# Kernel optimization log

Measured on AMD Instinct MI355X. Metric: run time of the kernel, lower is better.

The kernel has to match this reference:

```python
import jax, jax.numpy as jnp
import numpy as np

N = 8192      # num_nodes (adj.shape[0])
CIN = 32
COUT = 32     # must equal CIN so wd = x @ wp @ x.T is (N, N)
CS = 4        # Chebyshev order, static operator
CD = 4        # Chebyshev order, dynamic operator


def setup_inputs() -> dict:
    key = jax.random.key(0)
    k1, k2, k3, k4, k5 = jax.random.split(key, 5)
    x = jax.random.normal(k1, (N, CIN), jnp.float32)
    # scale ws so its spectral radius is O(1); keeps the Chebyshev recurrence numerically tame
    ws = jax.random.normal(k2, (N, N), jnp.float32) * np.float32(1.0 / np.sqrt(N))
    # small scale on wp so wd = x wp x^T has O(1) entries
    wp = jax.random.normal(k3, (CIN, COUT), jnp.float32) * np.float32(1e-3)
    ts = jax.random.normal(k4, (CS, CIN, COUT), jnp.float32)
    td = jax.random.normal(k5, (CD, CIN, COUT), jnp.float32)
    return {"x": x, "ws": ws, "wp": wp, "ts": ts, "td": td}


def reference(x, ws, wp, ts, td):
    # Static operator: Chebyshev expansion T0 = I, T1 = ws, Tk = 2 ws T_{k-1} - T_{k-2}.
    # Run the recurrence on the propagated features y_k = T_k(ws) @ x  (N, cin)
    # instead of forming the (N, N) polynomial matrices -- same math, far less traffic.
    y0 = x                      # T0 @ x
    y1 = ws @ x                 # T1 @ x
    out = y0 @ ts[0]            # shared k=0 term (added into both branches, as in the source)
    out_s = out + y1 @ ts[1]
    for k in range(2, CS):
        y0, y1 = y1, 2.0 * (ws @ y1) - y0
        out_s = out_s + y1 @ ts[k]
    # Dynamic operator: data-dependent graph wd = x @ wp @ x.T  (N, N)
    wd = (x @ wp) @ x.T
    z0 = x
    z1 = wd @ x
    out_d = out + z1 @ td[1]
    for k in range(2, CD):
        z0, z1 = z1, 2.0 * (wd @ z1) - z0
        out_d = out_d + z1 @ td[k]
    # act_func is None in this configuration
    return out_s + out_d
```

## Files before the change

kernel.cpp:

```cpp
#include <hip/hip_runtime.h>
#include <hip/hip_bf16.h>


typedef __attribute__((ext_vector_type(8))) short short8;
typedef __attribute__((ext_vector_type(4))) float floatx4;

__device__ inline unsigned short f2bf(float f) {
    union { float f; unsigned u; } v; v.f = f;
    unsigned r = v.u + 0x7FFFu + ((v.u >> 16) & 1u);
    return (unsigned short)(r >> 16);
}

__global__ __launch_bounds__(256) void k_prep(const float* __restrict__ x,
                                              const float* __restrict__ wp,
                                              float* __restrict__ xp,
                                              float* __restrict__ Gpart,
                                              unsigned short* __restrict__ Vt) {
    __shared__ float sx[8192];
    __shared__ float swp[1024];
    __shared__ unsigned short st[32][264];
    const int t = threadIdx.x;
    const int n0 = blockIdx.x * 256;
    const floatx4* x4 = (const floatx4*)(x + (size_t)n0 * 32);
    floatx4* sx4 = (floatx4*)sx;
#pragma unroll
    for (int i = 0; i < 8; ++i) sx4[i * 256 + t] = x4[i * 256 + t];
    for (int i = t; i < 1024; i += 256) swp[i] = wp[i];
    __syncthreads();

    float row[32];
#pragma unroll
    for (int a = 0; a < 32; ++a) row[a] = sx[t * 32 + a];

    float* xpr = xp + (size_t)(n0 + t) * 32;
#pragma unroll
    for (int c = 0; c < 32; ++c) {
        float s = 0.f;
#pragma unroll
        for (int a = 0; a < 32; ++a) s += row[a] * swp[a * 32 + c];
        xpr[c] = s;
        st[c][t] = f2bf(row[c]);
    }

    const int a = t >> 3;
    const int b = 4 * (t & 7);
    float g0 = 0.f, g1 = 0.f, g2 = 0.f, g3 = 0.f;
    for (int i = 0; i < 256; ++i) {
        float va = sx[i * 32 + a];
        floatx4 vb = *(floatx4*)&sx[i * 32 + b];
        g0 += va * vb.x; g1 += va * vb.y; g2 += va * vb.z; g3 += va * vb.w;
    }
    floatx4 g = {g0, g1, g2, g3};
    *(floatx4*)&Gpart[(size_t)blockIdx.x * 1024 + (size_t)(a * 32 + b)] = g;

    __syncthreads();
#pragma unroll
    for (int c = 0; c < 32; ++c) Vt[(size_t)c * 8192 + n0 + t] = st[c][t];
}

__global__ void k_coef(const float* __restrict__ Gpart, const float* __restrict__ wp,
                       const float* __restrict__ ts, const float* __restrict__ td,
                       float* __restrict__ Cx, float* __restrict__ Cxp) {
    __shared__ float G[1024], W[1024], H1[1024], H2[1024];
    __shared__ float swp[1024], td1[1024], td2[1024], td3[1024], ts0[1024];
    int t = threadIdx.x;
    int a = t >> 5, b = t & 31;
    float gs = 0.f;
    for (int p = 0; p < 32; ++p) gs += Gpart[p * 1024 + t];
    G[t] = gs; swp[t] = wp[t]; ts0[t] = ts[t];
    td1[t] = td[1024 + t]; td2[t] = td[2048 + t]; td3[t] = td[3072 + t];
    __syncthreads();
    float s = 0.f;
    for (int c = 0; c < 32; ++c) s += G[a * 32 + c] * swp[c * 32 + b];
    W[t] = s; __syncthreads();
    s = 0.f;
    for (int c = 0; c < 32; ++c) s += W[a * 32 + c] * G[c * 32 + b];
    H1[t] = s; __syncthreads();
    s = 0.f;
    for (int c = 0; c < 32; ++c) s += W[a * 32 + c] * H1[c * 32 + b];
    H2[t] = 2.f * s - G[t]; __syncthreads();
    s = 0.f;
    for (int c = 0; c < 32; ++c)
        s += G[a * 32 + c] * td1[c * 32 + b]
           + 2.f * H1[a * 32 + c] * td2[c * 32 + b]
           + (2.f * H2[a * 32 + c] - G[a * 32 + c]) * td3[c * 32 + b];
    Cxp[t] = s;
    Cx[t] = 2.f * ts0[t] - td2[t];
}

template <bool CONV>
__global__ __launch_bounds__(256) void k_gemm(const float* __restrict__ Af,
                                              const unsigned short* __restrict__ Ab,
                                              unsigned short* __restrict__ wsb_out,
                                              const unsigned short* __restrict__ Vt,
                                              float* __restrict__ Ypart) {
    const int t = threadIdx.x;
    const int lane = t & 63;
    const int wv = t >> 6;
    const int l15 = lane & 15;
    const int l4 = lane >> 4;
    const int m0 = blockIdx.x * 64;
    const int k0 = blockIdx.y * 1024;

    floatx4 acc0 = {0.f, 0.f, 0.f, 0.f};
    floatx4 acc1 = {0.f, 0.f, 0.f, 0.f};

    if (CONV) {
        __shared__ float sm[64 * 64];
        for (int kt = 0; kt < 1024; kt += 64) {
            __syncthreads();
#pragma unroll
            for (int i = 0; i < 4; ++i) {
                int r = i * 16 + (t >> 4);
                int j = t & 15;
                int cch = j ^ (r & 15);
                const float* gsrc = Af + (size_t)(m0 + r) * 8192 + (k0 + kt) + cch * 4;
                float* ldst = &sm[(i * 16 + wv * 4) * 64];
                __builtin_amdgcn_global_load_lds(
                    (const __attribute__((address_space(1))) unsigned int*)gsrc,
                    (__attribute__((address_space(3))) unsigned int*)ldst, 16, 0, 0);
            }
            __syncthreads();
#pragma unroll
            for (int kh = 0; kh < 2; ++kh) {
                int rl = wv * 16 + l15;
                int jb = kh * 8 + l4 * 2;
                floatx4 f0 = *(floatx4*)&sm[rl * 64 + ((jb    ) ^ l15) * 4];
                floatx4 f1 = *(floatx4*)&sm[rl * 64 + ((jb + 1) ^ l15) * 4];
                short8 av;
                av[0] = f2bf(f0.x); av[1] = f2bf(f0.y); av[2] = f2bf(f0.z); av[3] = f2bf(f0.w);
                av[4] = f2bf(f1.x); av[5] = f2bf(f1.y); av[6] = f2bf(f1.z); av[7] = f2bf(f1.w);
                int kk = k0 + kt + kh * 32 + l4 * 8;
                *(short8*)(wsb_out + (size_t)(m0 + rl) * 8192 + kk) = av;
                short8 b0 = *(const short8*)(Vt + (size_t)l15 * 8192 + kk);
                short8 b1 = *(const short8*)(Vt + (size_t)(16 + l15) * 8192 + kk);
                acc0 = __builtin_amdgcn_mfma_f32_16x16x32_bf16(av, b0, acc0, 0, 0, 0);
                acc1 = __builtin_amdgcn_mfma_f32_16x16x32_bf16(av, b1, acc1, 0, 0, 0);
            }
        }
    } else {
        __shared__ unsigned short sm16[64 * 64];
        for (int kt = 0; kt < 1024; kt += 64) {
            __syncthreads();
#pragma unroll
            for (int i = 0; i < 2; ++i) {
                int r = i * 32 + (t >> 3);
                int j = t & 7;
                int cch = j ^ (r & 7);
                const unsigned short* gsrc =
                    Ab + (size_t)(m0 + r) * 8192 + (k0 + kt) + cch * 8;
                unsigned short* ldst = &sm16[(i * 32 + wv * 8) * 64];
                __builtin_amdgcn_global_load_lds(
                    (const __attribute__((address_space(1))) unsigned int*)gsrc,
                    (__attribute__((address_space(3))) unsigned int*)ldst, 16, 0, 0);
            }
            __syncthreads();
#pragma unroll
            for (int kh = 0; kh < 2; ++kh) {
                int rl = wv * 16 + l15;
                short8 av = *(short8*)&sm16[rl * 64 + ((kh * 4 + l4) ^ (rl & 7)) * 8];
                int kk = k0 + kt + kh * 32 + l4 * 8;
                short8 b0 = *(const short8*)(Vt + (size_t)l15 * 8192 + kk);
                short8 b1 = *(const short8*)(Vt + (size_t)(16 + l15) * 8192 + kk);
                acc0 = __builtin_amdgcn_mfma_f32_16x16x32_bf16(av, b0, acc0, 0, 0, 0);
                acc1 = __builtin_amdgcn_mfma_f32_16x16x32_bf16(av, b1, acc1, 0, 0, 0);
            }
        }
    }
    float* yp = Ypart + (size_t)blockIdx.y * 262144;
    int row0 = m0 + wv * 16 + l4 * 4;
#pragma unroll
    for (int i = 0; i < 4; ++i) {
        yp[(size_t)(row0 + i) * 32 + l15] = acc0[i];
        yp[(size_t)(row0 + i) * 32 + 16 + l15] = acc1[i];
    }
}

__global__ __launch_bounds__(256) void k_trans(const float* __restrict__ Ypart,
                                               const float* __restrict__ prev,
                                               float alpha, float beta,
                                               float* __restrict__ y,
                                               unsigned short* __restrict__ Vt) {
    __shared__ unsigned short st[32][264];
    const int t = threadIdx.x;
    const int n0 = blockIdx.x * 256;
    const size_t base4 = (size_t)n0 * 8;
    floatx4 r[8];
#pragma unroll
    for (int j = 0; j < 8; ++j) r[j] = {0.f, 0.f, 0.f, 0.f};
    for (int p = 0; p < 8; ++p) {
        const floatx4* P4 = (const floatx4*)(Ypart + (size_t)p * 262144);
#pragma unroll
        for (int j = 0; j < 8; ++j) r[j] += P4[base4 + j * 256 + t];
    }
    const floatx4* prev4 = (const floatx4*)prev;
    floatx4* y4 = (floatx4*)y;
#pragma unroll
    for (int j = 0; j < 8; ++j) {
        floatx4 pv = prev4[base4 + j * 256 + t];
        floatx4 v;
        v.x = alpha * r[j].x + beta * pv.x;
        v.y = alpha * r[j].y + beta * pv.y;
        v.z = alpha * r[j].z + beta * pv.z;
        v.w = alpha * r[j].w + beta * pv.w;
        y4[base4 + j * 256 + t] = v;
        int q = j * 256 + t;
        int lr = q >> 3;
        int c4 = (q & 7) * 4;
        st[c4 + 0][lr] = f2bf(v.x);
        st[c4 + 1][lr] = f2bf(v.y);
        st[c4 + 2][lr] = f2bf(v.z);
        st[c4 + 3][lr] = f2bf(v.w);
    }
    __syncthreads();
#pragma unroll
    for (int c = 0; c < 32; ++c) Vt[(size_t)c * 8192 + n0 + t] = st[c][t];
}

__global__ void k_final(const float* __restrict__ x, const float* __restrict__ xp,
                        const float* __restrict__ y1, const float* __restrict__ y2,
                        const float* __restrict__ y3, const float* __restrict__ Cx,
                        const float* __restrict__ Cxp, const float* __restrict__ ts,
                        float* __restrict__ out) {
    __shared__ float m0[1024], m1[1024], m2[1024], m3[1024], m4[1024];
    int t = threadIdx.x;
    for (int i = t; i < 1024; i += 256) {
        m0[i] = Cx[i]; m1[i] = Cxp[i];
        m2[i] = ts[1024 + i]; m3[i] = ts[2048 + i]; m4[i] = ts[3072 + i];
    }
    __syncthreads();
    int g = blockIdx.x * 256 + t;
    int n = g >> 5, c = g & 31;
    const float* xr  = x  + (size_t)n * 32;
    const float* xpr = xp + (size_t)n * 32;
    const float* y1r = y1 + (size_t)n * 32;
    const float* y2r = y2 + (size_t)n * 32;
    const float* y3r = y3 + (size_t)n * 32;
    float s = 0.f;
#pragma unroll
    for (int a = 0; a < 32; ++a) {
        s += xr[a]  * m0[a * 32 + c]
           + xpr[a] * m1[a * 32 + c]
           + y1r[a] * m2[a * 32 + c]
           + y2r[a] * m3[a * 32 + c]
           + y3r[a] * m4[a * 32 + c];
    }
    out[g] = s;
}

extern "C" void kernel_launch(void* const* d_in, const int* in_sizes, int n_in,
                              void* d_out, int out_size, void* d_ws, size_t ws_size,
                              hipStream_t stream) {
    const float* x  = (const float*)d_in[0];
    const float* ws = (const float*)d_in[1];
    const float* wp = (const float*)d_in[2];
    const float* ts = (const float*)d_in[3];
    const float* td = (const float*)d_in[4];
    float* out = (float*)d_out;

    char* w = (char*)d_ws;
    unsigned short* wsb = (unsigned short*)w;
    float* Ppart = (float*)(w + 134217728);
    float* xp  = Ppart + 2097152;
    float* y1  = xp + 262144;
    float* y2  = y1 + 262144;
    float* y3  = y2 + 262144;
    unsigned short* Vt = (unsigned short*)(y3 + 262144);
    float* Gpart = (float*)(Vt + 262144);
    float* Cx  = Gpart + 32768;
    float* Cxp = Cx + 1024;

    dim3 gg(128, 8);
    k_prep<<<32, 256, 0, stream>>>(x, wp, xp, Gpart, Vt);
    k_coef<<<1, 1024, 0, stream>>>(Gpart, wp, ts, td, Cx, Cxp);
    k_gemm<true><<<gg, 256, 0, stream>>>(ws, nullptr, wsb, Vt, Ppart);
    k_trans<<<32, 256, 0, stream>>>(Ppart, x, 1.0f, 0.0f, y1, Vt);
    k_gemm<false><<<gg, 256, 0, stream>>>(nullptr, wsb, nullptr, Vt, Ppart);
    k_trans<<<32, 256, 0, stream>>>(Ppart, x, 2.0f, -1.0f, y2, Vt);
    k_gemm<false><<<gg, 256, 0, stream>>>(nullptr, wsb, nullptr, Vt, Ppart);
    k_trans<<<32, 256, 0, stream>>>(Ppart, y1, 2.0f, -1.0f, y3, Vt);

    k_final<<<1024, 256, 0, stream>>>(x, xp, y1, y2, y3, Cx, Cxp, ts, out);
}
```

Baseline: 567.3 us.

## Store bf16 ws in MFMA-fragment order and drop LDS staging in GEMMs

The first GEMM now reads fp32 ws rows directly from global memory with no LDS or barriers, converts them to bf16, and writes them out in a per-block, per-wave fragment-ordered layout. The later GEMMs can then load each lane's A fragment as one fully coalesced 16-byte read with no shared memory. The K split is doubled to 16 to raise the number of blocks in flight. In exchange, the reduction kernel reads twice as many partial buffers, and the fp32 row reads in the first GEMM are strided rather than cooperatively staged.

```diff
diff --git a/kernel.cpp b/kernel.cpp
--- a/kernel.cpp
+++ b/kernel.cpp
@@ -4,6 +4,9 @@
 
 typedef __attribute__((ext_vector_type(8))) short short8;
 typedef __attribute__((ext_vector_type(4))) float floatx4;
+
+constexpr int NSPLIT = 16;
+constexpr int KT_PER = 8;
 
 __device__ inline unsigned short f2bf(float f) {
     union { float f; unsigned u; } v; v.f = f;
@@ -88,91 +91,91 @@
     Cx[t] = 2.f * ts0[t] - td2[t];
 }
 
-template <bool CONV>
-__global__ __launch_bounds__(256) void k_gemm(const float* __restrict__ Af,
-                                              const unsigned short* __restrict__ Ab,
-                                              unsigned short* __restrict__ wsb_out,
-                                              const unsigned short* __restrict__ Vt,
-                                              float* __restrict__ Ypart) {
+__global__ __launch_bounds__(256) void k_gemm1(const float* __restrict__ A,
+                                               unsigned short* __restrict__ wsb,
+                                               const unsigned short* __restrict__ Vt,
+                                               float* __restrict__ Ypart) {
     const int t = threadIdx.x;
     const int lane = t & 63;
     const int wv = t >> 6;
     const int l15 = lane & 15;
     const int l4 = lane >> 4;
-    const int m0 = blockIdx.x * 64;
-    const int k0 = blockIdx.y * 1024;
+    const int bx = blockIdx.x, by = blockIdx.y;
+    const int k0 = by * 512;
+    const int row = bx * 64 + wv * 16 + l15;
+
+    const float* arow = A + (size_t)row * 8192 + k0 + l4 * 8;
+    unsigned short* wout =
+        wsb + (((size_t)(bx * NSPLIT + by) * 4096) + (size_t)wv * 64 + lane) * 8;
+    const unsigned short* vb0 = Vt + (size_t)l15 * 8192 + k0 + l4 * 8;
+    const unsigned short* vb1 = vb0 + (size_t)16 * 8192;
 
     floatx4 acc0 = {0.f, 0.f, 0.f, 0.f};
     floatx4 acc1 = {0.f, 0.f, 0.f, 0.f};
 
-    if (CONV) {
-        __shared__ float sm[64 * 64];
-        for (int kt = 0; kt < 1024; kt += 64) {
-            __syncthreads();
-#pragma unroll
-            for (int i = 0; i < 4; ++i) {
-                int r = i * 16 + (t >> 4);
-                int j = t & 15;
-                int cch = j ^ (r & 15);
-                const float* gsrc = Af + (size_t)(m0 + r) * 8192 + (k0 + kt) + cch * 4;
-                float* ldst = &sm[(i * 16 + wv * 4) * 64];
-                __builtin_amdgcn_global_load_lds(
-                    (const __attribute__((address_space(1))) unsigned int*)gsrc,
-                    (__attribute__((address_space(3))) unsigned int*)ldst, 16, 0, 0);
-            }
-            __syncthreads();
-#pragma unroll
-            for (int kh = 0; kh < 2; ++kh) {
-                int rl = wv * 16 + l15;
-                int jb = kh * 8 + l4 * 2;
-                floatx4 f0 = *(floatx4*)&sm[rl * 64 + ((jb    ) ^ l15) * 4];
-                floatx4 f1 = *(floatx4*)&sm[rl * 64 + ((jb + 1) ^ l15) * 4];
-                short8 av;
-                av[0] = f2bf(f0.x); av[1] = f2bf(f0.y); av[2] = f2bf(f0.z); av[3] = f2bf(f0.w);
-                av[4] = f2bf(f1.x); av[5] = f2bf(f1.y); av[6] = f2bf(f1.z); av[7] = f2bf(f1.w);
-                int kk = k0 + kt + kh * 32 + l4 * 8;
-                *(short8*)(wsb_out + (size_t)(m0 + rl) * 8192 + kk) = av;
-                short8 b0 = *(const short8*)(Vt + (size_t)l15 * 8192 + kk);
-                short8 b1 = *(const short8*)(Vt + (size_t)(16 + l15) * 8192 + kk);
-                acc0 = __builtin_amdgcn_mfma_f32_16x16x32_bf16(av, b0, acc0, 0, 0, 0);
-                acc1 = __builtin_amdgcn_mfma_f32_16x16x32_bf16(av, b1, acc1, 0, 0, 0);
-            }
+#pragma unroll
+    for (int kt = 0; kt < KT_PER; ++kt) {
+#pragma unroll
+        for (int i = 0; i < 2; ++i) {
+            const int kk = kt * 64 + i * 32;
+            floatx4 f0 = *(const floatx4*)(arow + kk);
+            floatx4 f1 = *(const floatx4*)(arow + kk + 4);
+            short8 av;
+            av[0] = f2bf(f0.x); av[1] = f2bf(f0.y); av[2] = f2bf(f0.z); av[3] = f2bf(f0.w);
+            av[4] = f2bf(f1.x); av[5] = f2bf(f1.y); av[6] = f2bf(f1.z); av[7] = f2bf(f1.w);
+            *(short8*)(wout + (size_t)(kt * 2 + i) * 2048) = av;
+            short8 b0 = *(const short8*)(vb0 + kk);
+            short8 b1 = *(const short8*)(vb1 + kk);
+            acc0 = __builtin_amdgcn_mfma_f32_16x16x32_bf16(av, b0, acc0, 0, 0, 0);
+            acc1 = __builtin_amdgcn_mfma_f32_16x16x32_bf16(av, b1, acc1, 0, 0, 0);
         }
-    } else {
-        __shared__ unsigned short sm16[64 * 64];
-        for (int kt = 0; kt < 1024; kt += 64) {
-            __syncthreads();
-#pragma unroll
-            for (int i = 0; i < 2; ++i) {
-                int r = i * 32 + (t >> 3);
-                int j = t & 7;
-                int cch = j ^ (r & 7);
-                const unsigned short* gsrc =
-                    Ab + (size_t)(m0 + r) * 8192 + (k0 + kt) + cch * 8;
-                unsigned short* ldst = &sm16[(i * 32 + wv * 8) * 64];
-                __builtin_amdgcn_global_load_lds(
-                    (const __attribute__((address_space(1))) unsigned int*)gsrc,
-                    (__attribute__((address_space(3))) unsigned int*)ldst, 16, 0, 0);
-            }
-            __syncthreads();
-#pragma unroll
-            for (int kh = 0; kh < 2; ++kh) {
-                int rl = wv * 16 + l15;
-                short8 av = *(short8*)&sm16[rl * 64 + ((kh * 4 + l4) ^ (rl & 7)) * 8];
-                int kk = k0 + kt + kh * 32 + l4 * 8;
-                short8 b0 = *(const short8*)(Vt + (size_t)l15 * 8192 + kk);
-                short8 b1 = *(const short8*)(Vt + (size_t)(16 + l15) * 8192 + kk);
-                acc0 = __builtin_amdgcn_mfma_f32_16x16x32_bf16(av, b0, acc0, 0, 0, 0);
-                acc1 = __builtin_amdgcn_mfma_f32_16x16x32_bf16(av, b1, acc1, 0, 0, 0);
-            }
+    }
+    float* yp = Ypart + (size_t)by * 262144;
+    const int row0 = bx * 64 + wv * 16 + l4 * 4;
+#pragma unroll
+    for (int r = 0; r < 4; ++r) {
+        yp[(size_t)(row0 + r) * 32 + l15] = acc0[r];
+        yp[(size_t)(row0 + r) * 32 + 16 + l15] = acc1[r];
+    }
+}
+
+__global__ __launch_bounds__(256) void k_gemm2(const unsigned short* __restrict__ wsb,
+                                               const unsigned short* __restrict__ Vt,
+                                               float* __restrict__ Ypart) {
+    const int t = threadIdx.x;
+    const int lane = t & 63;
+    const int wv = t >> 6;
+    const int l15 = lane & 15;
+    const int l4 = lane >> 4;
+    const int bx = blockIdx.x, by = blockIdx.y;
+    const int k0 = by * 512;
+
+    const short8* win = (const short8*)wsb
+        + ((size_t)(bx * NSPLIT + by) * 4096) + (size_t)wv * 64 + lane;
+    const unsigned short* vb0 = Vt + (size_t)l15 * 8192 + k0 + l4 * 8;
+    const unsigned short* vb1 = vb0 + (size_t)16 * 8192;
+
+    floatx4 acc0 = {0.f, 0.f, 0.f, 0.f};
+    floatx4 acc1 = {0.f, 0.f, 0.f, 0.f};
+
+#pragma unroll
+    for (int kt = 0; kt < KT_PER; ++kt) {
+#pragma unroll
+        for (int i = 0; i < 2; ++i) {
+            const int kk = kt * 64 + i * 32;
+            short8 av = win[(size_t)(kt * 2 + i) * 256];
+            short8 b0 = *(const short8*)(vb0 + kk);
+            short8 b1 = *(const short8*)(vb1 + kk);
+            acc0 = __builtin_amdgcn_mfma_f32_16x16x32_bf16(av, b0, acc0, 0, 0, 0);
+            acc1 = __builtin_amdgcn_mfma_f32_16x16x32_bf16(av, b1, acc1, 0, 0, 0);
         }
     }
-    float* yp = Ypart + (size_t)blockIdx.y * 262144;
-    int row0 = m0 + wv * 16 + l4 * 4;
-#pragma unroll
-    for (int i = 0; i < 4; ++i) {
-        yp[(size_t)(row0 + i) * 32 + l15] = acc0[i];
-        yp[(size_t)(row0 + i) * 32 + 16 + l15] = acc1[i];
+    float* yp = Ypart + (size_t)by * 262144;
+    const int row0 = bx * 64 + wv * 16 + l4 * 4;
+#pragma unroll
+    for (int r = 0; r < 4; ++r) {
+        yp[(size_t)(row0 + r) * 32 + l15] = acc0[r];
+        yp[(size_t)(row0 + r) * 32 + 16 + l15] = acc1[r];
     }
 }
 
@@ -188,7 +191,7 @@
     floatx4 r[8];
 #pragma unroll
     for (int j = 0; j < 8; ++j) r[j] = {0.f, 0.f, 0.f, 0.f};
-    for (int p = 0; p < 8; ++p) {
+    for (int p = 0; p < NSPLIT; ++p) {
         const floatx4* P4 = (const floatx4*)(Ypart + (size_t)p * 262144);
 #pragma unroll
         for (int j = 0; j < 8; ++j) r[j] += P4[base4 + j * 256 + t];
@@ -261,7 +264,7 @@
     char* w = (char*)d_ws;
     unsigned short* wsb = (unsigned short*)w;
     float* Ppart = (float*)(w + 134217728);
-    float* xp  = Ppart + 2097152;
+    float* xp  = Ppart + (size_t)NSPLIT * 262144;
     float* y1  = xp + 262144;
     float* y2  = y1 + 262144;
     float* y3  = y2 + 262144;
@@ -270,14 +273,14 @@
     float* Cx  = Gpart + 32768;
     float* Cxp = Cx + 1024;
 
-    dim3 gg(128, 8);
+    dim3 gg(128, NSPLIT);
     k_prep<<<32, 256, 0, stream>>>(x, wp, xp, Gpart, Vt);
     k_coef<<<1, 1024, 0, stream>>>(Gpart, wp, ts, td, Cx, Cxp);
-    k_gemm<true><<<gg, 256, 0, stream>>>(ws, nullptr, wsb, Vt, Ppart);
+    k_gemm1<<<gg, 256, 0, stream>>>(ws, wsb, Vt, Ppart);
     k_trans<<<32, 256, 0, stream>>>(Ppart, x, 1.0f, 0.0f, y1, Vt);
-    k_gemm<false><<<gg, 256, 0, stream>>>(nullptr, wsb, nullptr, Vt, Ppart);
+    k_gemm2<<<gg, 256, 0, stream>>>(wsb, Vt, Ppart);
     k_trans<<<32, 256, 0, stream>>>(Ppart, x, 2.0f, -1.0f, y2, Vt);
-    k_gemm<false><<<gg, 256, 0, stream>>>(nullptr, wsb, nullptr, Vt, Ppart);
+    k_gemm2<<<gg, 256, 0, stream>>>(wsb, Vt, Ppart);
     k_trans<<<32, 256, 0, stream>>>(Ppart, y1, 2.0f, -1.0f, y3, Vt);
 
     k_final<<<1024, 256, 0, stream>>>(x, xp, y1, y2, y3, Cx, Cxp, ts, out);
```

Result: faster. 541.6 us (-4.5%).
